# Optimization experiments

Measured on AMD Instinct MI355X. Metric: run time of the kernel, lower is better.

The kernel has to match this reference:

```python
import jax, jax.numpy as jnp
import numpy as np

B, C, T, H, W = 8, 512, 8, 28, 28
DI, DO = 256, 512  # dim_inner, dim_out
INIT_STD = 0.01
BN_EPS = 1e-5


def conv1x1(x, w, b):
    # 1x1x1 Conv3d == channel contraction. x: [B,C,T,H,W], w: [O,C], b: [O]
    return jnp.einsum('bcthw,oc->bothw', x, w) + b[None, :, None, None, None]


def setup_inputs() -> dict:
    key = jax.random.key(0)
    ks = jax.random.split(key, 8)
    x = jax.random.normal(ks[0], (B, C, T, H, W), jnp.float32)
    theta_w = INIT_STD * jax.random.normal(ks[1], (DI, C), jnp.float32)
    phi_w = INIT_STD * jax.random.normal(ks[2], (DI, C), jnp.float32)
    g_w = INIT_STD * jax.random.normal(ks[3], (DI, C), jnp.float32)
    out_w = INIT_STD * jax.random.normal(ks[4], (DO, DI), jnp.float32)
    theta_b = jnp.zeros((DI,), jnp.float32)
    phi_b = jnp.zeros((DI,), jnp.float32)
    g_b = jnp.zeros((DI,), jnp.float32)
    out_b = jnp.zeros((DO,), jnp.float32)
    bn_gamma = jnp.ones((DO,), jnp.float32)  # BN_INIT_GAMMA = 1.0
    bn_beta = jnp.zeros((DO,), jnp.float32)
    return {"x": x, "theta_w": theta_w, "theta_b": theta_b, "phi_w": phi_w,
            "phi_b": phi_b, "g_w": g_w, "g_b": g_b, "out_w": out_w,
            "out_b": out_b, "bn_gamma": bn_gamma, "bn_beta": bn_beta}


def reference(x, theta_w, theta_b, phi_w, phi_b, g_w, g_b, out_w, out_b, bn_gamma, bn_beta):
    b, c, t, h, w = x.shape
    scale = DI ** (-0.5)
    # theta on full resolution
    theta = conv1x1(x, theta_w, theta_b).reshape(b, DI, -1)          # [B,DI,N]
    # MaxPool3d((1,2,2)) with stride (1,2,2): H,W even -> block max
    mp = x.reshape(b, c, t, h // 2, 2, w // 2, 2).max(axis=(4, 6))   # [B,C,T,H/2,W/2]
    phi = conv1x1(mp, phi_w, phi_b).reshape(b, DI, -1)               # [B,DI,M]
    g = conv1x1(mp, g_w, g_b).reshape(b, DI, -1)                     # [B,DI,M]
    # attention: theta^T phi -> [B,N,M], scaled softmax over M
    logits = jnp.einsum('bdn,bdm->bnm', theta, phi) * scale
    p = jax.nn.softmax(logits, axis=-1)
    # t = g @ p^T -> [B,DI,N]
    tt = jnp.einsum('bdm,bnm->bdn', g, p).reshape(b, DI, t, h, w)
    out = conv1x1(tt, out_w, out_b)                                  # [B,DO,T,H,W]
    # BatchNorm3d (training-mode batch statistics over B,T,H,W)
    mean = out.mean(axis=(0, 2, 3, 4), keepdims=True)
    var = out.var(axis=(0, 2, 3, 4), keepdims=True)
    out = (out - mean) * jax.lax.rsqrt(var + BN_EPS)
    out = out * bn_gamma[None, :, None, None, None] + bn_beta[None, :, None, None, None]
    return out + x
```

## Files before the change

### kernel.cpp

```cpp
#include <hip/hip_runtime.h>
#include <hip/hip_bf16.h>

#define B_ 8
#define C_ 512
#define T_ 8
#define H_ 28
#define W_ 28
#define N_ (T_*H_*W_)
#define HP_ 14
#define WP_ 14
#define M_ (T_*HP_*WP_)
#define DI_ 256
#define DO_ 512
#define BN_EPS 1e-5f
#define SCALE_LOG2E 0.090168440055560214f
#define PSUM_COLS 392
#define PG_BS 425984
#define Q_SCALE 32768.0f
#define Q_INV   3.0517578125e-05f

typedef __attribute__((ext_vector_type(8))) short short8;
typedef __attribute__((ext_vector_type(4))) short short4v;
typedef __attribute__((ext_vector_type(4))) float float4v;
typedef __attribute__((ext_vector_type(16))) float float16v;
typedef __attribute__((ext_vector_type(2))) float float2v;

__device__ inline unsigned short f2bf(float f) {
    union { float f; unsigned int u; } v; v.f = f;
    unsigned int u = v.u;
    return (unsigned short)((u + 0x7FFFu + ((u >> 16) & 1u)) >> 16);
}
__device__ inline float bf2f(unsigned short h) {
    union { unsigned int u; float f; } v; v.u = ((unsigned int)h) << 16;
    return v.f;
}
__device__ inline void blockbar() {
    asm volatile("" ::: "memory");
    __builtin_amdgcn_s_barrier();
    asm volatile("" ::: "memory");
}

__global__ void xpose_x(const float* __restrict__ x, unsigned short* __restrict__ xT) {
    __shared__ float tile[64][65];
    int b = blockIdx.z;
    int c0 = blockIdx.y * 64, n0 = blockIdx.x * 64;
    const float* src = x + (size_t)b * C_ * N_;
    int tx = threadIdx.x & 63, ty = threadIdx.x >> 6;
#pragma unroll
    for (int i = 0; i < 16; i++) {
        int c = ty + i * 4;
        tile[c][tx] = src[(size_t)(c0 + c) * N_ + n0 + tx];
    }
    __syncthreads();
    unsigned short* d = xT + ((size_t)b * N_ + n0) * C_ + c0;
#pragma unroll
    for (int i = 0; i < 16; i++) {
        int n = ty + i * 4;
        d[(size_t)n * C_ + tx] = f2bf(tile[tx][n]);
    }
}

__global__ void pool_xpose(const float* __restrict__ x, unsigned short* __restrict__ mpT) {
    __shared__ unsigned short tile[196][72];
    int b = blockIdx.z, t = blockIdx.y, c0 = blockIdx.x * 64;
    const float* src = x + (((size_t)b * C_ + c0) * T_ + t) * 784;
    for (int idx = threadIdx.x; idx < 64 * 196; idx += 256) {
        int cc = idx / 196, p = idx - cc * 196;
        int hp = p / 14, wp = p - hp * 14;
        const float* r0 = src + (size_t)cc * T_ * 784 + (2 * hp) * 28 + 2 * wp;
        float2v a = *(const float2v*)r0;
        float2v c = *(const float2v*)(r0 + 28);
        float m = fmaxf(fmaxf(a.x, a.y), fmaxf(c.x, c.y));
        tile[p][cc] = f2bf(m);
    }
    __syncthreads();
    unsigned short* d = mpT + ((size_t)b * M_ + t * 196) * C_ + c0;
    for (int idx = threadIdx.x; idx < 196 * 64; idx += 256) {
        int p = idx >> 6, cc = idx & 63;
        d[(size_t)p * C_ + cc] = tile[p][cc];
    }
}

__global__ void cast_w4(const float* __restrict__ a0, const float* __restrict__ a1,
                        const float* __restrict__ a2, const float* __restrict__ a3,
                        unsigned short* __restrict__ d0, unsigned short* __restrict__ d1,
                        unsigned short* __restrict__ d2, unsigned short* __restrict__ d3) {
    int i = blockIdx.x * 256 + threadIdx.x;
    const float* s; unsigned short* d;
    switch (blockIdx.y) {
        case 0: s = a0; d = d0; break;
        case 1: s = a1; d = d1; break;
        case 2: s = a2; d = d2; break;
        default: s = a3; d = d3; break;
    }
    d[i] = f2bf(s[i]);
}

template<int GL>
__global__ __launch_bounds__(256, 2) void proj_gemm(
        const unsigned short* __restrict__ A, int MR,
        const unsigned short* __restrict__ W,
        unsigned short* __restrict__ Dp, size_t dBatch,
        const float* __restrict__ bias) {
    __shared__ __align__(16) unsigned short wqs[2][32][512];
    __shared__ __align__(16) unsigned short gscr[GL ? 4096 : 4];
    const int bid = blockIdx.x;
    const int b = bid & 7;
    const int nblk = bid >> 3;
    const int wave = threadIdx.x >> 6, lane = threadIdx.x & 63;
    const int lr = lane & 15, lk = lane >> 4;
    const unsigned short* Ab = A + (size_t)b * MR * C_;
    const int rbase = nblk * 128 + wave * 32;

    short8 a[2][16];
#pragma unroll
    for (int i = 0; i < 2; i++) {
        int row = rbase + i * 16 + lr; if (row >= MR) row = MR - 1;
#pragma unroll
        for (int kd = 0; kd < 16; kd++)
            a[i][kd] = *(const short8*)(Ab + (size_t)row * C_ + kd * 32 + lk * 8);
    }

    auto stage = [&](int bufi, int t) {
#pragma unroll
        for (int j = 0; j < 8; j++) {
            int row = wave * 8 + j;
            int qq = (lane * 16) ^ ((row & 7) << 4);
            const unsigned short* src = W + (size_t)(t * 32 + row) * C_ + (qq >> 1);
            unsigned short* dst = &wqs[bufi][0][0] + row * 512;
            __builtin_amdgcn_global_load_lds(
                (const __attribute__((address_space(1))) unsigned int*)src,
                (__attribute__((address_space(3))) unsigned int*)dst, 16, 0, 0);
        }
    };

    stage(0, 0);
    const int hq = (lk * 16) ^ ((lr & 7) << 4);
    unsigned short* Dlin = Dp + (size_t)b * dBatch + (size_t)rbase * DI_;
    unsigned short* Dg = Dp + (size_t)b * dBatch;
    int buf = 0;
#pragma unroll
    for (int t = 0; t < 8; t++) {
        if (t < 7) {
            stage(buf ^ 1, t + 1);
            if (t == 0) { asm volatile("s_waitcnt vmcnt(8)" ::: "memory"); }
            else if (GL == 0) { asm volatile("s_waitcnt vmcnt(24)" ::: "memory"); }
            else { asm volatile("s_waitcnt vmcnt(10)" ::: "memory"); }
        } else {
            if (GL == 0) { asm volatile("s_waitcnt vmcnt(16)" ::: "memory"); }
            else { asm volatile("s_waitcnt vmcnt(2)" ::: "memory"); }
        }
        blockbar();
        const char* Wb = (const char*)&wqs[buf][0][0];
        float4v acc[2][2] = {};
#pragma unroll
        for (int kd = 0; kd < 16; kd++) {
            short8 b0 = *(const short8*)(Wb + lr * 1024 + ((kd * 64) ^ hq));
            short8 b1 = *(const short8*)(Wb + (16 + lr) * 1024 + ((kd * 64) ^ hq));
            acc[0][0] = __builtin_amdgcn_mfma_f32_16x16x32_bf16(a[0][kd], b0, acc[0][0], 0, 0, 0);
            acc[0][1] = __builtin_amdgcn_mfma_f32_16x16x32_bf16(a[0][kd], b1, acc[0][1], 0, 0, 0);
            acc[1][0] = __builtin_amdgcn_mfma_f32_16x16x32_bf16(a[1][kd], b0, acc[1][0], 0, 0, 0);
            acc[1][1] = __builtin_amdgcn_mfma_f32_16x16x32_bf16(a[1][kd], b1, acc[1][1], 0, 0, 0);
        }
        if (GL == 0) {
#pragma unroll
            for (int i = 0; i < 2; i++)
#pragma unroll
                for (int j = 0; j < 2; j++) {
                    int col = t * 32 + j * 16 + lr;
                    float bv = bias[col];
#pragma unroll
                    for (int r = 0; r < 4; r++) {
                        int row = i * 16 + lk * 4 + r;
                        Dlin[(size_t)row * DI_ + col] = f2bf(acc[i][j][r] + bv);
                    }
                }
        } else {
#pragma unroll
            for (int i = 0; i < 2; i++) {
                int sm = (i * 2 + (lk >> 1)) & 3;
#pragma unroll
                for (int j = 0; j < 2; j++) {
                    int dd = j * 16 + lr;
                    int slot = dd * 4 + (sm ^ ((dd >> 3) & 3));
                    float bv = bias[t * 32 + dd];
                    short4v pk;
#pragma unroll
                    for (int r = 0; r < 4; r++) pk[r] = (short)f2bf(acc[i][j][r] + bv);
                    *(short4v*)(&gscr[wave * 1024 + slot * 8 + (lk & 1) * 4]) = pk;
                }
            }
            asm volatile("s_waitcnt lgkmcnt(0)" ::: "memory");
            blockbar();
#pragma unroll
            for (int r2 = 0; r2 < 2; r2++) {
                int idx = r2 * 256 + threadIdx.x;
                int w = idx >> 7;
                int o2 = (idx * 8) & 1023;
                short8 v = *(const short8*)(&gscr[idx * 8]);
                *(short8*)(Dg + (size_t)(nblk * 4 + w) * 8192 + t * 1024 + o2) = v;
            }
        }
        blockbar();
        buf ^= 1;
    }
}

__global__ __launch_bounds__(256, 2) void out_gemm(
        const unsigned short* __restrict__ wo,
        const unsigned short* __restrict__ Bh, const unsigned short* __restrict__ Bl,
        unsigned short* __restrict__ Dp, const float* __restrict__ bias,
        float* __restrict__ psum) {
    __shared__ __align__(16) unsigned short tts[2][2][32][256];
    const int bid = blockIdx.x;
    const int b = bid & 7;
    const int rem = bid >> 3;
    const int doblk = rem & 3;
    const int nchunk = rem >> 2;
    const int wave = threadIdx.x >> 6, lane = threadIdx.x & 63;
    const int lr = lane & 15, lk = lane >> 4;
    const unsigned short* Ab = wo + (size_t)(doblk * 128 + wave * 32) * DI_;
    const unsigned short* BhB = Bh + ((size_t)b * N_ + nchunk * 128) * DI_;
    const unsigned short* BlB = Bl + ((size_t)b * N_ + nchunk * 128) * DI_;

    short8 a[2][8];
#pragma unroll
    for (int i = 0; i < 2; i++)
#pragma unroll
        for (int kd = 0; kd < 8; kd++)
            a[i][kd] = *(const short8*)(Ab + (size_t)(i * 16 + lr) * DI_ + kd * 32 + lk * 8);

    auto stage = [&](int bufi, int t) {
#pragma unroll
        for (int p = 0; p < 2; p++) {
            const unsigned short* S = p ? BlB : BhB;
#pragma unroll
            for (int j = 0; j < 4; j++) {
                int chunk = wave * 4 + j;
                int row = chunk * 2 + (lane >> 5);
                int qq = (((lane & 31) * 16)) ^ ((row & 7) << 4);
                const unsigned short* src = S + (size_t)(t * 32 + row) * DI_ + (qq >> 1);
                unsigned short* dst = &tts[bufi][p][0][0] + chunk * 512;
                __builtin_amdgcn_global_load_lds(
                    (const __attribute__((address_space(1))) unsigned int*)src,
                    (__attribute__((address_space(3))) unsigned int*)dst, 16, 0, 0);
            }
        }
    };

    stage(0, 0);
    const int hq = (lk * 16) ^ ((lr & 7) << 4);
    float4v acc[4][2][2] = {};
    int buf = 0;
#pragma unroll
    for (int t = 0; t < 4; t++) {
        if (t < 3) {
            stage(buf ^ 1, t + 1);
            asm volatile("s_waitcnt vmcnt(8)" ::: "memory");
        } else {
            asm volatile("s_waitcnt vmcnt(0)" ::: "memory");
        }
        blockbar();
        const char* th = (const char*)&tts[buf][0][0][0];
        const char* tl = (const char*)&tts[buf][1][0][0];
#pragma unroll
        for (int kd = 0; kd < 8; kd++) {
            short8 bh0 = *(const short8*)(th + lr * 512 + ((kd * 64) ^ hq));
            short8 bh1 = *(const short8*)(th + (16 + lr) * 512 + ((kd * 64) ^ hq));
            short8 bl0 = *(const short8*)(tl + lr * 512 + ((kd * 64) ^ hq));
            short8 bl1 = *(const short8*)(tl + (16 + lr) * 512 + ((kd * 64) ^ hq));
            acc[t][0][0] = __builtin_amdgcn_mfma_f32_16x16x32_bf16(a[0][kd], bh0, acc[t][0][0], 0, 0, 0);
            acc[t][0][0] = __builtin_amdgcn_mfma_f32_16x16x32_bf16(a[0][kd], bl0, acc[t][0][0], 0, 0, 0);
            acc[t][0][1] = __builtin_amdgcn_mfma_f32_16x16x32_bf16(a[0][kd], bh1, acc[t][0][1], 0, 0, 0);
            acc[t][0][1] = __builtin_amdgcn_mfma_f32_16x16x32_bf16(a[0][kd], bl1, acc[t][0][1], 0, 0, 0);
            acc[t][1][0] = __builtin_amdgcn_mfma_f32_16x16x32_bf16(a[1][kd], bh0, acc[t][1][0], 0, 0, 0);
            acc[t][1][0] = __builtin_amdgcn_mfma_f32_16x16x32_bf16(a[1][kd], bl0, acc[t][1][0], 0, 0, 0);
            acc[t][1][1] = __builtin_amdgcn_mfma_f32_16x16x32_bf16(a[1][kd], bh1, acc[t][1][1], 0, 0, 0);
            acc[t][1][1] = __builtin_amdgcn_mfma_f32_16x16x32_bf16(a[1][kd], bl1, acc[t][1][1], 0, 0, 0);
        }
        blockbar();
        buf ^= 1;
    }
    unsigned short* Db = Dp + (size_t)b * DO_ * N_;
    float s1[2][4] = {}, s2[2][4] = {};
#pragma unroll
    for (int t = 0; t < 4; t++)
#pragma unroll
        for (int i = 0; i < 2; i++)
#pragma unroll
            for (int r = 0; r < 4; r++) {
                int dorow = doblk * 128 + wave * 32 + i * 16 + lk * 4 + r;
                float bv = bias[dorow];
                float v0 = acc[t][i][0][r] + bv;
                float v1 = acc[t][i][1][r] + bv;
                int ncol = nchunk * 128 + t * 32 + lr;
                float c0 = fminf(fmaxf(v0 * Q_SCALE, -32767.f), 32767.f);
                float c1 = fminf(fmaxf(v1 * Q_SCALE, -32767.f), 32767.f);
                Db[(size_t)dorow * N_ + ncol] = (unsigned short)(short)lrintf(c0);
                Db[(size_t)dorow * N_ + ncol + 16] = (unsigned short)(short)lrintf(c1);
                s1[i][r] += v0 + v1;
                s2[i][r] += v0 * v0 + v1 * v1;
            }
#pragma unroll
    for (int m = 1; m < 16; m <<= 1)
#pragma unroll
        for (int i = 0; i < 2; i++)
#pragma unroll
            for (int r = 0; r < 4; r++) {
                s1[i][r] += __shfl_xor(s1[i][r], m, 64);
                s2[i][r] += __shfl_xor(s2[i][r], m, 64);
            }
    if (lr == 0) {
        int pcol = b * 49 + nchunk;
#pragma unroll
        for (int i = 0; i < 2; i++)
#pragma unroll
            for (int r = 0; r < 4; r++) {
                int row = doblk * 128 + wave * 32 + i * 16 + lk * 4 + r;
                psum[(size_t)row * PSUM_COLS + pcol] = s1[i][r];
                psum[(size_t)(DO_ + row) * PSUM_COLS + pcol] = s2[i][r];
            }
    }
}

__global__ __launch_bounds__(256, 2) void attn_k(
        const unsigned short* __restrict__ thetaT,
        const unsigned short* __restrict__ phiT,
        const unsigned short* __restrict__ g,
        unsigned short* __restrict__ ttH,
        unsigned short* __restrict__ ttL) {
    __shared__ __align__(16) unsigned short phi_s[2][32][256];
    __shared__ __align__(16) unsigned short g_s[2][8192];
    const int bid = blockIdx.x;
    const int b = bid & 7;
    const int nblk = bid >> 3;
    const int wave = threadIdx.x >> 6, lane = threadIdx.x & 63;
    const int l31 = lane & 31, hi = lane >> 5;
    const int n0 = nblk * 128 + wave * 32;
    const unsigned short* Q  = thetaT + ((size_t)b * N_ + n0) * DI_;
    const unsigned short* Pg = phiT + (size_t)b * PG_BS;
    const unsigned short* G  = g + (size_t)b * PG_BS;

    short8 q[16];
#pragma unroll
    for (int kb = 0; kb < 16; kb++)
        q[kb] = *(const short8*)(Q + (size_t)l31 * DI_ + kb * 16 + hi * 8);

    float16v acc[8] = {};
    float rs = 0.f;

    auto stage = [&](int bufi, int t) {
        const unsigned short* phiRow = Pg + (size_t)t * 32 * DI_;
#pragma unroll
        for (int j = 0; j < 4; j++) {
            int chunk = wave * 4 + j;
            int row = chunk * 2 + (lane >> 5);
            int qq = ((lane & 31) * 16) ^ ((row & 31) << 4);
            const unsigned short* src = phiRow + (size_t)row * DI_ + (qq >> 1);
            unsigned short* dst = &phi_s[bufi][0][0] + chunk * 512;
            __builtin_amdgcn_global_load_lds(
                (const __attribute__((address_space(1))) unsigned int*)src,
                (__attribute__((address_space(3))) unsigned int*)dst, 16, 0, 0);
        }
        const unsigned short* Gt = G + (size_t)t * 8192;
#pragma unroll
        for (int j = 0; j < 4; j++) {
            int chunk = wave * 4 + j;
            const unsigned short* src = Gt + chunk * 512 + lane * 8;
            unsigned short* dst = &g_s[bufi][0] + chunk * 512;
            __builtin_amdgcn_global_load_lds(
                (const __attribute__((address_space(1))) unsigned int*)src,
                (__attribute__((address_space(3))) unsigned int*)dst, 16, 0, 0);
        }
    };

    stage(0, 0);
    const int pswz = l31 << 4;
    const int glow = hi ^ ((l31 >> 3) & 3);
    const int goff0 = (l31 * 4 + glow) << 4;
    const int goff1 = goff0 ^ 32;
    int buf = 0;
    const int NT = M_ / 32;
    for (int t = 0; t < NT; t++) {
        if (t + 1 < NT) {
            stage(buf ^ 1, t + 1);
            asm volatile("s_waitcnt vmcnt(8)" ::: "memory");
        } else {
            asm volatile("s_waitcnt vmcnt(0)" ::: "memory");
        }
        blockbar();

        const char* phiB = (const char*)&phi_s[buf][0][0];
        float16v S0 = {}, S1 = {};
        __builtin_amdgcn_s_setprio(1);
#pragma unroll
        for (int kb = 0; kb < 8; kb++) {
            short8 pha0 = *(const short8*)(phiB + l31 * 512 + ((kb * 32 + hi * 16) ^ pswz));
            short8 pha1 = *(const short8*)(phiB + l31 * 512 + (((kb + 8) * 32 + hi * 16) ^ pswz));
            S0 = __builtin_amdgcn_mfma_f32_32x32x16_bf16(pha0, q[kb], S0, 0, 0, 0);
            S1 = __builtin_amdgcn_mfma_f32_32x32x16_bf16(pha1, q[kb + 8], S1, 0, 0, 0);
        }
        __builtin_amdgcn_s_setprio(0);

        float p[16];
#pragma unroll
        for (int r = 0; r < 16; r++) {
            p[r] = exp2f((S0[r] + S1[r]) * SCALE_LOG2E);
            rs += p[r];
        }
        unsigned int pk0, pk1, pk2, pk3, pk4, pk5, pk6, pk7;
        asm("v_cvt_pk_bf16_f32 %0, %1, %2" : "=v"(pk0) : "v"(p[0]),  "v"(p[1]));
        asm("v_cvt_pk_bf16_f32 %0, %1, %2" : "=v"(pk1) : "v"(p[2]),  "v"(p[3]));
        asm("v_cvt_pk_bf16_f32 %0, %1, %2" : "=v"(pk2) : "v"(p[4]),  "v"(p[5]));
        asm("v_cvt_pk_bf16_f32 %0, %1, %2" : "=v"(pk3) : "v"(p[6]),  "v"(p[7]));
        asm("v_cvt_pk_bf16_f32 %0, %1, %2" : "=v"(pk4) : "v"(p[8]),  "v"(p[9]));
        asm("v_cvt_pk_bf16_f32 %0, %1, %2" : "=v"(pk5) : "v"(p[10]), "v"(p[11]));
        asm("v_cvt_pk_bf16_f32 %0, %1, %2" : "=v"(pk6) : "v"(p[12]), "v"(p[13]));
        asm("v_cvt_pk_bf16_f32 %0, %1, %2" : "=v"(pk7) : "v"(p[14]), "v"(p[15]));
        asm("v_permlane32_swap_b32 %0, %1" : "+v"(pk0), "+v"(pk2));
        asm("v_permlane32_swap_b32 %0, %1" : "+v"(pk1), "+v"(pk3));
        asm("v_permlane32_swap_b32 %0, %1" : "+v"(pk4), "+v"(pk6));
        asm("v_permlane32_swap_b32 %0, %1" : "+v"(pk5), "+v"(pk7));
        union UF { unsigned int u[4]; short8 s; } pa0, pa1;
        pa0.u[0] = pk0; pa0.u[1] = pk1; pa0.u[2] = pk2; pa0.u[3] = pk3;
        pa1.u[0] = pk4; pa1.u[1] = pk5; pa1.u[2] = pk6; pa1.u[3] = pk7;

        const char* gB = (const char*)&g_s[buf][0];
        __builtin_amdgcn_s_setprio(1);
#pragma unroll
        for (int dblk = 0; dblk < 8; dblk++) {
            short8 gb0 = *(const short8*)(gB + dblk * 2048 + goff0);
            short8 gb1 = *(const short8*)(gB + dblk * 2048 + goff1);
            acc[dblk] = __builtin_amdgcn_mfma_f32_32x32x16_bf16(pa0.s, gb0, acc[dblk], 0, 0, 0);
            acc[dblk] = __builtin_amdgcn_mfma_f32_32x32x16_bf16(pa1.s, gb1, acc[dblk], 0, 0, 0);
        }
        __builtin_amdgcn_s_setprio(0);
        blockbar();
        buf ^= 1;
    }

    rs += __shfl_xor(rs, 32, 64);
    float inv = 1.0f / rs;

    unsigned short* OH = ttH + ((size_t)b * N_ + n0) * DI_;
    unsigned short* OL = ttL + ((size_t)b * N_ + n0) * DI_;
#pragma unroll
    for (int reg = 0; reg < 16; reg++) {
        int n_l = (reg & 3) + 8 * (reg >> 2) + 4 * hi;
        float invn = __shfl(inv, n_l, 64);
#pragma unroll
        for (int dblk = 0; dblk < 8; dblk++) {
            float v = acc[dblk][reg] * invn;
            unsigned short h = f2bf(v);
            unsigned short l = f2bf(v - bf2f(h));
            size_t idx = (size_t)n_l * DI_ + dblk * 32 + l31;
            OH[idx] = h;
            OL[idx] = l;
        }
    }
}

__global__ void bn_finalize(const float* __restrict__ psum, float* __restrict__ stats) {
    int o = blockIdx.x;
    float s = 0.f, q = 0.f;
    for (int c = threadIdx.x; c < PSUM_COLS; c += 256) {
        s += psum[(size_t)o * PSUM_COLS + c];
        q += psum[(size_t)(DO_ + o) * PSUM_COLS + c];
    }
#pragma unroll
    for (int m = 1; m < 64; m <<= 1) { s += __shfl_xor(s, m, 64); q += __shfl_xor(q, m, 64); }
    __shared__ float ws1[4], ws2[4];
    int wave = threadIdx.x >> 6;
    if ((threadIdx.x & 63) == 0) { ws1[wave] = s; ws2[wave] = q; }
    __syncthreads();
    if (threadIdx.x == 0) {
        double S = (double)ws1[0] + ws1[1] + ws1[2] + ws1[3];
        double Q = (double)ws2[0] + ws2[1] + ws2[2] + ws2[3];
        const double cnt = (double)(B_ * N_);
        double mean = S / cnt;
        double var = Q / cnt - mean * mean;
        stats[o] = (float)mean;
        stats[DO_ + o] = (float)(1.0 / sqrt(var + (double)BN_EPS));
    }
}

__global__ void bn_apply(const unsigned short* __restrict__ ob, const float* __restrict__ x,
                         const float* __restrict__ stats, const float* __restrict__ gamma,
                         const float* __restrict__ beta, float* __restrict__ out) {
    size_t i = ((size_t)blockIdx.x * 256 + threadIdx.x) * 8;
    short8 v8 = *(const short8*)(ob + i);
    int o = (int)((i / N_) % DO_);
    float mean = stats[o], rsig = stats[DO_ + o];
    float ga = gamma[o], be = beta[o];
    float4v x0 = *(const float4v*)(x + i);
    float4v x1 = *(const float4v*)(x + i + 4);
    float4v r0, r1;
#pragma unroll
    for (int j = 0; j < 4; j++) {
        r0[j] = ((float)(short)v8[j] * Q_INV - mean) * rsig * ga + be + x0[j];
        r1[j] = ((float)(short)v8[4 + j] * Q_INV - mean) * rsig * ga + be + x1[j];
    }
    *(float4v*)(out + i) = r0;
    *(float4v*)(out + i + 4) = r1;
}

extern "C" void kernel_launch(void* const* d_in, const int* in_sizes, int n_in,
                              void* d_out, int out_size, void* d_ws, size_t ws_size,
                              hipStream_t stream) {
    const float* x       = (const float*)d_in[0];
    const float* theta_w = (const float*)d_in[1];
    const float* theta_b = (const float*)d_in[2];
    const float* phi_w   = (const float*)d_in[3];
    const float* phi_b   = (const float*)d_in[4];
    const float* g_w     = (const float*)d_in[5];
    const float* g_b     = (const float*)d_in[6];
    const float* out_w   = (const float*)d_in[7];
    const float* out_b   = (const float*)d_in[8];
    const float* bn_g    = (const float*)d_in[9];
    const float* bn_b    = (const float*)d_in[10];
    float* out = (float*)d_out;

    char* ws = (char*)d_ws;
    size_t off = 0;
    auto alloc = [&](size_t bytes) { void* p = ws + off; off += (bytes + 255) & ~(size_t)255; return p; };
    unsigned short* xT     = (unsigned short*)alloc((size_t)B_ * N_ * C_ * 2);
    unsigned short* mpT    = (unsigned short*)alloc((size_t)B_ * M_ * C_ * 2);
    unsigned short* thetaT = (unsigned short*)alloc((size_t)B_ * N_ * DI_ * 2);
    unsigned short* phiT   = (unsigned short*)alloc((size_t)B_ * PG_BS * 2);
    unsigned short* gbuf   = (unsigned short*)alloc((size_t)B_ * PG_BS * 2);
    unsigned short* wq     = (unsigned short*)alloc((size_t)DI_ * C_ * 2);
    unsigned short* wp     = (unsigned short*)alloc((size_t)DI_ * C_ * 2);
    unsigned short* wg     = (unsigned short*)alloc((size_t)DI_ * C_ * 2);
    unsigned short* wo     = (unsigned short*)alloc((size_t)DO_ * DI_ * 2);
    float* stats           = (float*)alloc((size_t)DO_ * 2 * 4);
    float* psum            = (float*)alloc((size_t)DO_ * 2 * PSUM_COLS * 4);
    unsigned short* ttH    = xT;
    unsigned short* ttL    = xT + (size_t)B_ * N_ * DI_;
    unsigned short* out_q  = mpT;

    cast_w4<<<dim3(512, 4), 256, 0, stream>>>(theta_w, phi_w, g_w, out_w, wq, wp, wg, wo);

    xpose_x<<<dim3(N_ / 64, C_ / 64, B_), 256, 0, stream>>>(x, xT);
    pool_xpose<<<dim3(C_ / 64, T_, B_), 256, 0, stream>>>(x, mpT);

    proj_gemm<0><<<392, 256, 0, stream>>>(xT, N_, wq, thetaT, (size_t)N_ * DI_, theta_b);
    proj_gemm<0><<<104, 256, 0, stream>>>(mpT, M_, wp, phiT, (size_t)PG_BS, phi_b);
    proj_gemm<1><<<104, 256, 0, stream>>>(mpT, M_, wg, gbuf, (size_t)PG_BS, g_b);

    attn_k<<<dim3((N_ / 128) * 8), 256, 0, stream>>>(thetaT, phiT, gbuf, ttH, ttL);

    out_gemm<<<1568, 256, 0, stream>>>(wo, ttH, ttL, out_q, out_b, psum);

    bn_finalize<<<DO_, 256, 0, stream>>>(psum, stats);
    bn_apply<<<(size_t)B_ * DO_ * N_ / 8 / 256, 256, 0, stream>>>(out_q, x, stats, bn_g, bn_b, out);
}
```

Before: 323.1 us.

## Give each attention wave two query tiles and pool from bf16 transposed x

After: 356.3 us. +10.3%, slower.

```diff
diff --git a/kernel.cpp b/kernel.cpp
--- a/kernel.cpp
+++ b/kernel.cpp
@@ -60,25 +60,24 @@
     }
 }
 
-__global__ void pool_xpose(const float* __restrict__ x, unsigned short* __restrict__ mpT) {
-    __shared__ unsigned short tile[196][72];
-    int b = blockIdx.z, t = blockIdx.y, c0 = blockIdx.x * 64;
-    const float* src = x + (((size_t)b * C_ + c0) * T_ + t) * 784;
-    for (int idx = threadIdx.x; idx < 64 * 196; idx += 256) {
-        int cc = idx / 196, p = idx - cc * 196;
-        int hp = p / 14, wp = p - hp * 14;
-        const float* r0 = src + (size_t)cc * T_ * 784 + (2 * hp) * 28 + 2 * wp;
-        float2v a = *(const float2v*)r0;
-        float2v c = *(const float2v*)(r0 + 28);
-        float m = fmaxf(fmaxf(a.x, a.y), fmaxf(c.x, c.y));
-        tile[p][cc] = f2bf(m);
-    }
-    __syncthreads();
-    unsigned short* d = mpT + ((size_t)b * M_ + t * 196) * C_ + c0;
-    for (int idx = threadIdx.x; idx < 196 * 64; idx += 256) {
-        int p = idx >> 6, cc = idx & 63;
-        d[(size_t)p * C_ + cc] = tile[p][cc];
-    }
+__global__ void pool_from_xT(const unsigned short* __restrict__ xT, unsigned short* __restrict__ mpT) {
+    int b = blockIdx.y;
+    int p = blockIdx.x;
+    int t = p / 196, pp = p - t * 196;
+    int hp = pp / 14, wp = pp - hp * 14;
+    int n00 = t * 784 + (2 * hp) * 28 + 2 * wp;
+    const unsigned short* r0 = xT + ((size_t)b * N_ + n00) * C_;
+    int c = threadIdx.x * 2;
+    unsigned int a = *(const unsigned int*)(r0 + c);
+    unsigned int bb = *(const unsigned int*)(r0 + C_ + c);
+    unsigned int cc = *(const unsigned int*)(r0 + 28 * C_ + c);
+    unsigned int dd = *(const unsigned int*)(r0 + 29 * C_ + c);
+    float lo = fmaxf(fmaxf(bf2f(a & 0xFFFF), bf2f(bb & 0xFFFF)),
+                     fmaxf(bf2f(cc & 0xFFFF), bf2f(dd & 0xFFFF)));
+    float hi = fmaxf(fmaxf(bf2f(a >> 16), bf2f(bb >> 16)),
+                     fmaxf(bf2f(cc >> 16), bf2f(dd >> 16)));
+    unsigned int r = (unsigned int)f2bf(lo) | ((unsigned int)f2bf(hi) << 16);
+    *(unsigned int*)(mpT + ((size_t)b * M_ + p) * C_ + c) = r;
 }
 
 __global__ void cast_w4(const float* __restrict__ a0, const float* __restrict__ a1,
@@ -323,7 +322,7 @@
     }
 }
 
-__global__ __launch_bounds__(256, 2) void attn_k(
+__global__ __launch_bounds__(128, 1) void attn_k(
         const unsigned short* __restrict__ thetaT,
         const unsigned short* __restrict__ phiT,
         const unsigned short* __restrict__ g,
@@ -336,24 +335,26 @@
     const int nblk = bid >> 3;
     const int wave = threadIdx.x >> 6, lane = threadIdx.x & 63;
     const int l31 = lane & 31, hi = lane >> 5;
-    const int n0 = nblk * 128 + wave * 32;
+    const int n0 = nblk * 128 + wave * 64;
     const unsigned short* Q  = thetaT + ((size_t)b * N_ + n0) * DI_;
     const unsigned short* Pg = phiT + (size_t)b * PG_BS;
     const unsigned short* G  = g + (size_t)b * PG_BS;
 
-    short8 q[16];
-#pragma unroll
-    for (int kb = 0; kb < 16; kb++)
-        q[kb] = *(const short8*)(Q + (size_t)l31 * DI_ + kb * 16 + hi * 8);
-
-    float16v acc[8] = {};
-    float rs = 0.f;
+    short8 q0[16], q1[16];
+#pragma unroll
+    for (int kb = 0; kb < 16; kb++) {
+        q0[kb] = *(const short8*)(Q + (size_t)l31 * DI_ + kb * 16 + hi * 8);
+        q1[kb] = *(const short8*)(Q + (size_t)(32 + l31) * DI_ + kb * 16 + hi * 8);
+    }
+
+    float16v acc0[8] = {}, acc1[8] = {};
+    float rs0 = 0.f, rs1 = 0.f;
 
     auto stage = [&](int bufi, int t) {
         const unsigned short* phiRow = Pg + (size_t)t * 32 * DI_;
 #pragma unroll
-        for (int j = 0; j < 4; j++) {
-            int chunk = wave * 4 + j;
+        for (int j = 0; j < 8; j++) {
+            int chunk = wave * 8 + j;
             int row = chunk * 2 + (lane >> 5);
             int qq = ((lane & 31) * 16) ^ ((row & 31) << 4);
             const unsigned short* src = phiRow + (size_t)row * DI_ + (qq >> 1);
@@ -364,8 +365,8 @@
         }
         const unsigned short* Gt = G + (size_t)t * 8192;
 #pragma unroll
-        for (int j = 0; j < 4; j++) {
-            int chunk = wave * 4 + j;
+        for (int j = 0; j < 8; j++) {
+            int chunk = wave * 8 + j;
             const unsigned short* src = Gt + chunk * 512 + lane * 8;
             unsigned short* dst = &g_s[bufi][0] + chunk * 512;
             __builtin_amdgcn_global_load_lds(
@@ -384,7 +385,7 @@
     for (int t = 0; t < NT; t++) {
         if (t + 1 < NT) {
             stage(buf ^ 1, t + 1);
-            asm volatile("s_waitcnt vmcnt(8)" ::: "memory");
+            asm volatile("s_waitcnt vmcnt(16)" ::: "memory");
         } else {
             asm volatile("s_waitcnt vmcnt(0)" ::: "memory");
         }
@@ -394,36 +395,54 @@
         float16v S0 = {}, S1 = {};
         __builtin_amdgcn_s_setprio(1);
 #pragma unroll
-        for (int kb = 0; kb < 8; kb++) {
-            short8 pha0 = *(const short8*)(phiB + l31 * 512 + ((kb * 32 + hi * 16) ^ pswz));
-            short8 pha1 = *(const short8*)(phiB + l31 * 512 + (((kb + 8) * 32 + hi * 16) ^ pswz));
-            S0 = __builtin_amdgcn_mfma_f32_32x32x16_bf16(pha0, q[kb], S0, 0, 0, 0);
-            S1 = __builtin_amdgcn_mfma_f32_32x32x16_bf16(pha1, q[kb + 8], S1, 0, 0, 0);
+        for (int kb = 0; kb < 16; kb++) {
+            short8 pha = *(const short8*)(phiB + l31 * 512 + ((kb * 32 + hi * 16) ^ pswz));
+            S0 = __builtin_amdgcn_mfma_f32_32x32x16_bf16(pha, q0[kb], S0, 0, 0, 0);
+            S1 = __builtin_amdgcn_mfma_f32_32x32x16_bf16(pha, q1[kb], S1, 0, 0, 0);
         }
         __builtin_amdgcn_s_setprio(0);
 
-        float p[16];
-#pragma unroll
-        for (int r = 0; r < 16; r++) {
-            p[r] = exp2f((S0[r] + S1[r]) * SCALE_LOG2E);
-            rs += p[r];
-        }
-        unsigned int pk0, pk1, pk2, pk3, pk4, pk5, pk6, pk7;
-        asm("v_cvt_pk_bf16_f32 %0, %1, %2" : "=v"(pk0) : "v"(p[0]),  "v"(p[1]));
-        asm("v_cvt_pk_bf16_f32 %0, %1, %2" : "=v"(pk1) : "v"(p[2]),  "v"(p[3]));
-        asm("v_cvt_pk_bf16_f32 %0, %1, %2" : "=v"(pk2) : "v"(p[4]),  "v"(p[5]));
-        asm("v_cvt_pk_bf16_f32 %0, %1, %2" : "=v"(pk3) : "v"(p[6]),  "v"(p[7]));
-        asm("v_cvt_pk_bf16_f32 %0, %1, %2" : "=v"(pk4) : "v"(p[8]),  "v"(p[9]));
-        asm("v_cvt_pk_bf16_f32 %0, %1, %2" : "=v"(pk5) : "v"(p[10]), "v"(p[11]));
-        asm("v_cvt_pk_bf16_f32 %0, %1, %2" : "=v"(pk6) : "v"(p[12]), "v"(p[13]));
-        asm("v_cvt_pk_bf16_f32 %0, %1, %2" : "=v"(pk7) : "v"(p[14]), "v"(p[15]));
-        asm("v_permlane32_swap_b32 %0, %1" : "+v"(pk0), "+v"(pk2));
-        asm("v_permlane32_swap_b32 %0, %1" : "+v"(pk1), "+v"(pk3));
-        asm("v_permlane32_swap_b32 %0, %1" : "+v"(pk4), "+v"(pk6));
-        asm("v_permlane32_swap_b32 %0, %1" : "+v"(pk5), "+v"(pk7));
-        union UF { unsigned int u[4]; short8 s; } pa0, pa1;
-        pa0.u[0] = pk0; pa0.u[1] = pk1; pa0.u[2] = pk2; pa0.u[3] = pk3;
-        pa1.u[0] = pk4; pa1.u[1] = pk5; pa1.u[2] = pk6; pa1.u[3] = pk7;
+        union UF { unsigned int u[4]; short8 s; } pa0s0, pa1s0, pa0s1, pa1s1;
+        {
+            float p[16];
+#pragma unroll
+            for (int r = 0; r < 16; r++) { p[r] = exp2f(S0[r] * SCALE_LOG2E); rs0 += p[r]; }
+            unsigned int k0, k1, k2, k3, k4, k5, k6, k7;
+            asm("v_cvt_pk_bf16_f32 %0, %1, %2" : "=v"(k0) : "v"(p[0]),  "v"(p[1]));
+            asm("v_cvt_pk_bf16_f32 %0, %1, %2" : "=v"(k1) : "v"(p[2]),  "v"(p[3]));
+            asm("v_cvt_pk_bf16_f32 %0, %1, %2" : "=v"(k2) : "v"(p[4]),  "v"(p[5]));
+            asm("v_cvt_pk_bf16_f32 %0, %1, %2" : "=v"(k3) : "v"(p[6]),  "v"(p[7]));
+            asm("v_cvt_pk_bf16_f32 %0, %1, %2" : "=v"(k4) : "v"(p[8]),  "v"(p[9]));
+            asm("v_cvt_pk_bf16_f32 %0, %1, %2" : "=v"(k5) : "v"(p[10]), "v"(p[11]));
+            asm("v_cvt_pk_bf16_f32 %0, %1, %2" : "=v"(k6) : "v"(p[12]), "v"(p[13]));
+            asm("v_cvt_pk_bf16_f32 %0, %1, %2" : "=v"(k7) : "v"(p[14]), "v"(p[15]));
+            asm("v_permlane32_swap_b32 %0, %1" : "+v"(k0), "+v"(k2));
+            asm("v_permlane32_swap_b32 %0, %1" : "+v"(k1), "+v"(k3));
+            asm("v_permlane32_swap_b32 %0, %1" : "+v"(k4), "+v"(k6));
+            asm("v_permlane32_swap_b32 %0, %1" : "+v"(k5), "+v"(k7));
+            pa0s0.u[0] = k0; pa0s0.u[1] = k1; pa0s0.u[2] = k2; pa0s0.u[3] = k3;
+            pa1s0.u[0] = k4; pa1s0.u[1] = k5; pa1s0.u[2] = k6; pa1s0.u[3] = k7;
+        }
+        {
+            float p[16];
+#pragma unroll
+            for (int r = 0; r < 16; r++) { p[r] = exp2f(S1[r] * SCALE_LOG2E); rs1 += p[r]; }
+            unsigned int k0, k1, k2, k3, k4, k5, k6, k7;
+            asm("v_cvt_pk_bf16_f32 %0, %1, %2" : "=v"(k0) : "v"(p[0]),  "v"(p[1]));
+            asm("v_cvt_pk_bf16_f32 %0, %1, %2" : "=v"(k1) : "v"(p[2]),  "v"(p[3]));
+            asm("v_cvt_pk_bf16_f32 %0, %1, %2" : "=v"(k2) : "v"(p[4]),  "v"(p[5]));
+            asm("v_cvt_pk_bf16_f32 %0, %1, %2" : "=v"(k3) : "v"(p[6]),  "v"(p[7]));
+            asm("v_cvt_pk_bf16_f32 %0, %1, %2" : "=v"(k4) : "v"(p[8]),  "v"(p[9]));
+            asm("v_cvt_pk_bf16_f32 %0, %1, %2" : "=v"(k5) : "v"(p[10]), "v"(p[11]));
+            asm("v_cvt_pk_bf16_f32 %0, %1, %2" : "=v"(k6) : "v"(p[12]), "v"(p[13]));
+            asm("v_cvt_pk_bf16_f32 %0, %1, %2" : "=v"(k7) : "v"(p[14]), "v"(p[15]));
+            asm("v_permlane32_swap_b32 %0, %1" : "+v"(k0), "+v"(k2));
+            asm("v_permlane32_swap_b32 %0, %1" : "+v"(k1), "+v"(k3));
+            asm("v_permlane32_swap_b32 %0, %1" : "+v"(k4), "+v"(k6));
+            asm("v_permlane32_swap_b32 %0, %1" : "+v"(k5), "+v"(k7));
+            pa0s1.u[0] = k0; pa0s1.u[1] = k1; pa0s1.u[2] = k2; pa0s1.u[3] = k3;
+            pa1s1.u[0] = k4; pa1s1.u[1] = k5; pa1s1.u[2] = k6; pa1s1.u[3] = k7;
+        }
 
         const char* gB = (const char*)&g_s[buf][0];
         __builtin_amdgcn_s_setprio(1);
@@ -431,31 +450,39 @@
         for (int dblk = 0; dblk < 8; dblk++) {
             short8 gb0 = *(const short8*)(gB + dblk * 2048 + goff0);
             short8 gb1 = *(const short8*)(gB + dblk * 2048 + goff1);
-            acc[dblk] = __builtin_amdgcn_mfma_f32_32x32x16_bf16(pa0.s, gb0, acc[dblk], 0, 0, 0);
-            acc[dblk] = __builtin_amdgcn_mfma_f32_32x32x16_bf16(pa1.s, gb1, acc[dblk], 0, 0, 0);
+            acc0[dblk] = __builtin_amdgcn_mfma_f32_32x32x16_bf16(pa0s0.s, gb0, acc0[dblk], 0, 0, 0);
+            acc1[dblk] = __builtin_amdgcn_mfma_f32_32x32x16_bf16(pa0s1.s, gb0, acc1[dblk], 0, 0, 0);
+            acc0[dblk] = __builtin_amdgcn_mfma_f32_32x32x16_bf16(pa1s0.s, gb1, acc0[dblk], 0, 0, 0);
+            acc1[dblk] = __builtin_amdgcn_mfma_f32_32x32x16_bf16(pa1s1.s, gb1, acc1[dblk], 0, 0, 0);
         }
         __builtin_amdgcn_s_setprio(0);
         blockbar();
         buf ^= 1;
     }
 
-    rs += __shfl_xor(rs, 32, 64);
-    float inv = 1.0f / rs;
-
-    unsigned short* OH = ttH + ((size_t)b * N_ + n0) * DI_;
-    unsigned short* OL = ttL + ((size_t)b * N_ + n0) * DI_;
-#pragma unroll
-    for (int reg = 0; reg < 16; reg++) {
-        int n_l = (reg & 3) + 8 * (reg >> 2) + 4 * hi;
-        float invn = __shfl(inv, n_l, 64);
-#pragma unroll
-        for (int dblk = 0; dblk < 8; dblk++) {
-            float v = acc[dblk][reg] * invn;
-            unsigned short h = f2bf(v);
-            unsigned short l = f2bf(v - bf2f(h));
-            size_t idx = (size_t)n_l * DI_ + dblk * 32 + l31;
-            OH[idx] = h;
-            OL[idx] = l;
+    rs0 += __shfl_xor(rs0, 32, 64);
+    rs1 += __shfl_xor(rs1, 32, 64);
+    float inv0 = 1.0f / rs0;
+    float inv1 = 1.0f / rs1;
+
+#pragma unroll
+    for (int set = 0; set < 2; set++) {
+        unsigned short* OH = ttH + ((size_t)b * N_ + n0 + set * 32) * DI_;
+        unsigned short* OL = ttL + ((size_t)b * N_ + n0 + set * 32) * DI_;
+        float inv = set ? inv1 : inv0;
+#pragma unroll
+        for (int reg = 0; reg < 16; reg++) {
+            int n_l = (reg & 3) + 8 * (reg >> 2) + 4 * hi;
+            float invn = __shfl(inv, n_l, 64);
+#pragma unroll
+            for (int dblk = 0; dblk < 8; dblk++) {
+                float v = (set ? acc1[dblk][reg] : acc0[dblk][reg]) * invn;
+                unsigned short h = f2bf(v);
+                unsigned short l = f2bf(v - bf2f(h));
+                size_t idx = (size_t)n_l * DI_ + dblk * 32 + l31;
+                OH[idx] = h;
+                OL[idx] = l;
+            }
         }
     }
 }
@@ -541,13 +568,13 @@
     cast_w4<<<dim3(512, 4), 256, 0, stream>>>(theta_w, phi_w, g_w, out_w, wq, wp, wg, wo);
 
     xpose_x<<<dim3(N_ / 64, C_ / 64, B_), 256, 0, stream>>>(x, xT);
-    pool_xpose<<<dim3(C_ / 64, T_, B_), 256, 0, stream>>>(x, mpT);
+    pool_from_xT<<<dim3(M_, B_), 256, 0, stream>>>(xT, mpT);
 
     proj_gemm<0><<<392, 256, 0, stream>>>(xT, N_, wq, thetaT, (size_t)N_ * DI_, theta_b);
     proj_gemm<0><<<104, 256, 0, stream>>>(mpT, M_, wp, phiT, (size_t)PG_BS, phi_b);
     proj_gemm<1><<<104, 256, 0, stream>>>(mpT, M_, wg, gbuf, (size_t)PG_BS, g_b);
 
-    attn_k<<<dim3((N_ / 128) * 8), 256, 0, stream>>>(thetaT, phiT, gbuf, ttH, ttL);
+    attn_k<<<dim3((N_ / 128) * 8), 128, 0, stream>>>(thetaT, phiT, gbuf, ttH, ttL);
 
     out_gemm<<<1568, 256, 0, stream>>>(wo, ttH, ttL, out_q, out_b, psum);
 
```
